# Kernel optimization log

Hardware: AMD Instinct MI355X
Metric: run time of the kernel (lower is better)

The kernel has to match this reference:

```python
import jax, jax.numpy as jnp
import numpy as np

IN, H, OUT = 128, 256, 128


def setup_inputs() -> dict:
    key = jax.random.key(0)
    ks = jax.random.split(key, 12)
    B, T = 32, 128
    s_in = 1.0 / np.sqrt(IN)
    s_h = 1.0 / np.sqrt(H)
    return {
        "x": jax.random.normal(ks[0], (B, T, IN), dtype=jnp.float32),
        "timespans": jax.random.uniform(ks[1], (B, T), dtype=jnp.float32),
        "tau_sys": jax.random.uniform(ks[2], (H,), dtype=jnp.float32) * 10.0 + 1.0,
        "sigma": jnp.ones((H,), dtype=jnp.float32) * 0.5,
        "W_A": jax.random.normal(ks[3], (H, H), dtype=jnp.float32) * s_h,
        "W_B": jax.random.normal(ks[4], (H, IN), dtype=jnp.float32) * s_in,
        "b_B": jax.random.normal(ks[5], (H,), dtype=jnp.float32) * s_in,
        "W_C": jax.random.normal(ks[6], (OUT, H), dtype=jnp.float32) * s_h,
        "b_C": jax.random.normal(ks[7], (OUT,), dtype=jnp.float32) * s_h,
        "W_ih": jax.random.normal(ks[8], (4 * H, IN), dtype=jnp.float32) * s_h,
        "W_hh": jax.random.normal(ks[9], (4 * H, H), dtype=jnp.float32) * s_h,
        "b_ih": jax.random.normal(ks[10], (4 * H,), dtype=jnp.float32) * s_h,
        "b_hh": jax.random.normal(ks[11], (4 * H,), dtype=jnp.float32) * s_h,
    }


def _lstm(x, W_ih, W_hh, b_ih, b_hh):
    # x: [B,T,IN] -> backbone_out: [B,T,H]; torch gate order i,f,g,o
    B = x.shape[0]
    xg = jnp.einsum("bti,gi->btg", x, W_ih) + b_ih  # precompute input contribution

    def step(carry, xg_t):
        h, c = carry
        gates = xg_t + h @ W_hh.T + b_hh
        i, f, g, o = jnp.split(gates, 4, axis=-1)
        c = jax.nn.sigmoid(f) * c + jax.nn.sigmoid(i) * jnp.tanh(g)
        h = jax.nn.sigmoid(o) * jnp.tanh(c)
        return (h, c), h

    h0 = jnp.zeros((B, H), dtype=x.dtype)
    c0 = jnp.zeros((B, H), dtype=x.dtype)
    _, hs = jax.lax.scan(step, (h0, c0), jnp.swapaxes(xg, 0, 1))
    return jnp.swapaxes(hs, 0, 1)  # [B,T,H]


def reference(x, timespans, tau_sys, sigma, W_A, W_B, b_B, W_C, b_C,
              W_ih, W_hh, b_ih, b_hh):
    B, T, _ = x.shape
    backbone_out = _lstm(x, W_ih, W_hh, b_ih, b_hh)  # [B,T,H]

    A_eff = W_A / tau_sys[None, :]        # [H,H] (divide columns, as in torch)
    I = jnp.eye(H, dtype=x.dtype)
    Bx = jnp.einsum("bti,hi->bth", x, W_B) + b_B  # precompute B(x_t) for all t

    def step(h, inp):
        x_t_Bx, bb_t, ts_t = inp  # [B,H], [B,H], [B]
        f_h = jnp.tanh(h / sigma)
        At = A_eff[None, :, :] * ts_t[:, None, None]            # [B,H,H]
        exp_At = I + At + 0.5 * jnp.einsum("bij,bjk->bik", At, At)
        h_new = jnp.einsum("bij,bj->bi", exp_At, h)
        drive = x_t_Bx + f_h @ W_A.T
        h_new = h_new + ts_t[:, None] * drive / tau_sys[None, :]
        h_new = h_new + bb_t
        y = h_new @ W_C.T + b_C
        return h_new, y

    h0 = jnp.zeros((B, H), dtype=x.dtype)
    xs = (jnp.swapaxes(Bx, 0, 1), jnp.swapaxes(backbone_out, 0, 1),
          jnp.swapaxes(timespans, 0, 1))
    _, ys = jax.lax.scan(step, h0, xs)
    return jnp.swapaxes(ys, 0, 1)  # [B,T,OUT]
```

## Files before the change

kernel.cpp:

```cpp
#include <hip/hip_runtime.h>
#include <math.h>

#define T_ 128

#define OFF_M2      0
#define OFF_WCOMBT  65536
#define OFF_BIAS    229376
#define OFF_WCT     230656
#define OFF_XG2     263424
#define OFF_BX2     4457728
#define OFF_HSEQ    5506304
#define OFF_HCSEQ   6554880

#define SENTB 0xFFFFFFFFu

typedef float f4 __attribute__((ext_vector_type(4)));

__device__ __forceinline__ float sigm_f(float x) { return 1.0f / (1.0f + __expf(-x)); }
__device__ __forceinline__ float tanh_f(float x) { return 1.0f - 2.0f / (__expf(2.0f * x) + 1.0f); }

__device__ __forceinline__ unsigned long long aload_u64(const unsigned long long* p) {
  return __hip_atomic_load(p, __ATOMIC_RELAXED, __HIP_MEMORY_SCOPE_AGENT);
}
__device__ __forceinline__ void astore_f(float* p, float v) {
  __hip_atomic_store(p, v, __ATOMIC_RELAXED, __HIP_MEMORY_SCOPE_AGENT);
}
__device__ __forceinline__ bool bad_u64(unsigned long long v) {
  return (unsigned)v == SENTB || (unsigned)(v >> 32) == SENTB;
}

__global__ __launch_bounds__(256) void prep_kernel(
    const float* __restrict__ W_ih, const float* __restrict__ W_B,
    const float* __restrict__ b_ih, const float* __restrict__ b_hh,
    const float* __restrict__ b_B,  const float* __restrict__ W_C,
    const float* __restrict__ W_A,  const float* __restrict__ tau,
    float* __restrict__ ws) {
  __shared__ float adrow[256];
  const int blk = blockIdx.x, tid = threadIdx.x;
  if (blk < 640) {
    const int idx = blk * 256 + tid;
    const int k = idx / 1280, c = idx - k * 1280;
    ws[OFF_WCOMBT + idx] = (c < 1024) ? W_ih[c * 128 + k] : W_B[(c - 1024) * 128 + k];
  } else if (blk == 640) {
#pragma unroll
    for (int i = 0; i < 5; ++i) {
      const int id = i * 256 + tid;
      ws[OFF_BIAS + id] = (id < 1024) ? (b_ih[id] + b_hh[id]) : b_B[id - 1024];
    }
  } else if (blk < 769) {
    const int idx = (blk - 641) * 256 + tid;
    const int k = idx >> 7, o = idx & 127;
    ws[OFF_WCT + idx] = W_C[o * 256 + k];
  } else if (blk < 1025) {
    const int i = blk - 769, k = tid;
    const float itk = 1.0f / tau[k];
    adrow[k] = W_A[i * 256 + k] * itk;
    __syncthreads();
    float s = 0.f;
#pragma unroll 8
    for (int m = 0; m < 256; ++m)
      s = fmaf(adrow[m], W_A[m * 256 + k], s);
    ws[OFF_M2 + i * 256 + k] = s * itk;
  } else {
    uint4* dst = (uint4*)(ws + OFF_HSEQ);
    const uint4 sv = make_uint4(SENTB, SENTB, SENTB, SENTB);
    const int tg = (blk - 1025) * 256 + tid;
#pragma unroll
    for (int i = 0; i < 16; ++i) dst[tg + i * 32768] = sv;
  }
}

__global__ __launch_bounds__(256) void xgt_kernel(
    const float* __restrict__ x, const float* __restrict__ WT,
    const float* __restrict__ bias, float* __restrict__ xg2,
    float* __restrict__ bx2) {
  __shared__ float xs[8 * 128];
  const int tid = threadIdx.x;
  const int rt = blockIdx.x, ct = blockIdx.y;
  ((float4*)xs)[tid] = ((const float4*)(x + rt * 1024))[tid];
  __syncthreads();
  const int r = tid >> 5, cg = tid & 31;
  const int c0 = ct * 256 + cg * 8;
  const float4* b4 = (const float4*)(bias + c0);
  float4 bA = b4[0], bB = b4[1];
  float a[8] = {bA.x, bA.y, bA.z, bA.w, bB.x, bB.y, bB.z, bB.w};
  const float4* xr4 = (const float4*)(xs + r * 128);
#pragma unroll 4
  for (int k4 = 0; k4 < 32; ++k4) {
    float4 xv = xr4[k4];
#define STEPB(kk, comp)                                                      \
    {                                                                        \
      const float4* w = (const float4*)(WT + (k4 * 4 + kk) * 1280 + c0);     \
      float4 wA = w[0], wB = w[1];                                           \
      a[0] = fmaf(wA.x, comp, a[0]); a[1] = fmaf(wA.y, comp, a[1]);          \
      a[2] = fmaf(wA.z, comp, a[2]); a[3] = fmaf(wA.w, comp, a[3]);          \
      a[4] = fmaf(wB.x, comp, a[4]); a[5] = fmaf(wB.y, comp, a[5]);          \
      a[6] = fmaf(wB.z, comp, a[6]); a[7] = fmaf(wB.w, comp, a[7]);          \
    }
    STEPB(0, xv.x) STEPB(1, xv.y) STEPB(2, xv.z) STEPB(3, xv.w)
#undef STEPB
  }
  const int row = rt * 8 + r;
  const int b = row >> 7, t = row & 127;
  if (ct < 4) {
    float* dst = xg2 + (size_t)(t * 32 + b) * 1024 + ct * 256 + cg * 8;
#pragma unroll
    for (int i = 0; i < 8; ++i) dst[i] = a[i];
  } else {
    float* dst = bx2 + (size_t)(t * 32 + b) * 256 + cg * 8;
#pragma unroll
    for (int i = 0; i < 8; ++i) dst[i] = a[i];
  }
}

__device__ __forceinline__ float wc_elem(
    const float* __restrict__ W_A, const float* __restrict__ M2,
    const float* __restrict__ tau, int ci, float it_i, int kp) {
  if (kp < 256)      return W_A[ci * 256 + kp] / tau[kp];
  else if (kp < 512) return W_A[ci * 256 + (kp - 256)] * it_i;
  else               return 0.5f * M2[ci * 256 + (kp - 512)];
}

__global__ __launch_bounds__(256, 4) void recur_bp_kernel(
    const float* __restrict__ ts_all, const float* __restrict__ tau,
    const float* __restrict__ sigma, const float* __restrict__ W_hh,
    const float* __restrict__ W_A, const float* __restrict__ M2,
    const float* __restrict__ xg2, const float* __restrict__ bx2,
    float* __restrict__ hseq, float* __restrict__ hcseq) {
  const int tid = threadIdx.x;
  const int lane = tid & 63, w = tid >> 6;
  const unsigned long long* hsq  = (const unsigned long long*)hseq;
  const unsigned long long* hcsq = (const unsigned long long*)hcseq;

  __shared__ float h_s[2][256];
  __shared__ float q_s[2][768];

  if (blockIdx.x < 512) {
    const int b = blockIdx.x >> 4, cb16 = blockIdx.x & 15;
    const int kq = lane & 3;
    const int gt = (lane >> 2) & 3;
    const int dim = cb16 * 16 + 4 * w + (lane >> 4);
    const int grow = gt * 256 + dim;
    const f4* wsrc = (const f4*)(W_hh + grow * 256);
    f4 wq0  = wsrc[0 * 4 + kq],  wq1  = wsrc[1 * 4 + kq];
    f4 wq2  = wsrc[2 * 4 + kq],  wq3  = wsrc[3 * 4 + kq];
    f4 wq4  = wsrc[4 * 4 + kq],  wq5  = wsrc[5 * 4 + kq];
    f4 wq6  = wsrc[6 * 4 + kq],  wq7  = wsrc[7 * 4 + kq];
    f4 wq8  = wsrc[8 * 4 + kq],  wq9  = wsrc[9 * 4 + kq];
    f4 wq10 = wsrc[10 * 4 + kq], wq11 = wsrc[11 * 4 + kq];
    f4 wq12 = wsrc[12 * 4 + kq], wq13 = wsrc[13 * 4 + kq];
    f4 wq14 = wsrc[14 * 4 + kq], wq15 = wsrc[15 * 4 + kq];
    asm volatile("" : "+v"(wq0), "+v"(wq1), "+v"(wq2), "+v"(wq3),
                      "+v"(wq4), "+v"(wq5), "+v"(wq6), "+v"(wq7),
                      "+v"(wq8), "+v"(wq9), "+v"(wq10), "+v"(wq11),
                      "+v"(wq12), "+v"(wq13), "+v"(wq14), "+v"(wq15));
    float c_reg = 0.f;
    const int dcol = dim;

    for (int t = 0; t < T_; ++t) {
      const int buf = t & 1;
      float xgi = 0.f, xgf = 0.f, xgg = 0.f, xgo = 0.f;
      if ((lane & 15) == 0) {
        const float* xp = xg2 + (size_t)(t * 32 + b) * 1024 + dcol;
        xgi = xp[0]; xgf = xp[256]; xgg = xp[512]; xgo = xp[768];
      }
      if (t == 0) {
        if (tid < 128) ((float2*)h_s[0])[tid] = make_float2(0.f, 0.f);
      } else if (tid < 128) {
        const unsigned long long* pp = hsq + (size_t)((t - 1) * 32 + b) * 128 + tid;
        unsigned long long v = aload_u64(pp);
        int spins = 0;
        while (bad_u64(v)) {
          if (++spins > 16) __builtin_amdgcn_s_sleep(1);
          v = aload_u64(pp);
        }
        union { unsigned long long u; float2 f; } H; H.u = v;
        ((float2*)h_s[buf])[tid] = H.f;
      }
      __syncthreads();

      const f4* h4 = (const f4*)h_s[buf];
      float s = 0.f;
#define LSTEP(i4, W)                                                         \
      {                                                                      \
        const f4 hv = h4[i4 * 4 + kq];                                       \
        s = fmaf(W.x, hv.x, s); s = fmaf(W.y, hv.y, s);                      \
        s = fmaf(W.z, hv.z, s); s = fmaf(W.w, hv.w, s);                      \
      }
      LSTEP(0, wq0)   LSTEP(1, wq1)   LSTEP(2, wq2)   LSTEP(3, wq3)
      LSTEP(4, wq4)   LSTEP(5, wq5)   LSTEP(6, wq6)   LSTEP(7, wq7)
      LSTEP(8, wq8)   LSTEP(9, wq9)   LSTEP(10, wq10) LSTEP(11, wq11)
      LSTEP(12, wq12) LSTEP(13, wq13) LSTEP(14, wq14) LSTEP(15, wq15)
#undef LSTEP
      s += __shfl_xor(s, 1); s += __shfl_xor(s, 2);
      const int base = lane & 48;
      const float gi = __shfl(s, base);
      const float gf = __shfl(s, base + 4);
      const float gg = __shfl(s, base + 8);
      const float go = __shfl(s, base + 12);
      if ((lane & 15) == 0) {
        const float i_ = sigm_f(gi + xgi);
        const float f_ = sigm_f(gf + xgf);
        const float g_ = tanh_f(gg + xgg);
        const float o_ = sigm_f(go + xgo);
        c_reg = fmaf(f_, c_reg, i_ * g_);
        const float ht = o_ * tanh_f(c_reg);
        astore_f(hseq + (size_t)(t * 32 + b) * 256 + dcol, ht);
      }
      (void)gt;
    }
  } else {
    const int bix = blockIdx.x - 512;
    const int b = bix >> 4, cb16 = bix & 15;
    const int r_in = lane >> 4, kq16 = lane & 15;
    const int ci = cb16 * 16 + 4 * w + r_in;
    const float it_i = 1.0f / tau[ci];
#define WCLOAD(i4)                                                           \
    (f4){wc_elem(W_A, M2, tau, ci, it_i, (i4 * 16 + kq16) * 4 + 0),          \
         wc_elem(W_A, M2, tau, ci, it_i, (i4 * 16 + kq16) * 4 + 1),          \
         wc_elem(W_A, M2, tau, ci, it_i, (i4 * 16 + kq16) * 4 + 2),          \
         wc_elem(W_A, M2, tau, ci, it_i, (i4 * 16 + kq16) * 4 + 3)}
    f4 wc0  = WCLOAD(0),  wc1  = WCLOAD(1),  wc2  = WCLOAD(2);
    f4 wc3  = WCLOAD(3),  wc4  = WCLOAD(4),  wc5  = WCLOAD(5);
    f4 wc6  = WCLOAD(6),  wc7  = WCLOAD(7),  wc8  = WCLOAD(8);
    f4 wc9  = WCLOAD(9),  wc10 = WCLOAD(10), wc11 = WCLOAD(11);
#undef WCLOAD
    asm volatile("" : "+v"(wc0), "+v"(wc1), "+v"(wc2), "+v"(wc3),
                      "+v"(wc4), "+v"(wc5), "+v"(wc6), "+v"(wc7),
                      "+v"(wc8), "+v"(wc9), "+v"(wc10), "+v"(wc11));
    float2 isg2 = make_float2(0.f, 0.f);
    if (tid < 128) isg2 = make_float2(1.0f / sigma[2 * tid], 1.0f / sigma[2 * tid + 1]);
    const bool fin = (kq16 == 0);

    for (int t = 0; t < T_; ++t) {
      const int buf = t & 1;
      const float ts = ts_all[b * T_ + t];
      float bx_v = 0.f;
      if (fin) bx_v = bx2[(size_t)(t * 32 + b) * 256 + ci];

      if (t == 0) {
        if (tid < 128) {
          const float2 z = make_float2(0.f, 0.f);
          ((float2*)h_s[0])[tid] = z;
          float2* qrow = (float2*)q_s[0];
          qrow[tid] = z; qrow[128 + tid] = z; qrow[256 + tid] = z;
        }
      } else if (tid < 128) {
        const size_t base = (size_t)((t - 1) * 32 + b) * 128 + tid;
        const unsigned long long* pc = hcsq + base;
        const unsigned long long* ph = hsq + base;
        unsigned long long vc = aload_u64(pc);
        unsigned long long vh = aload_u64(ph);
        int spins = 0;
        while (bad_u64(vc) || bad_u64(vh)) {
          if (++spins > 16) __builtin_amdgcn_s_sleep(1);
          vc = aload_u64(pc);
          vh = aload_u64(ph);
        }
        union { unsigned long long u; float2 f; } C, H;
        C.u = vc; H.u = vh;
        const float2 hcv = make_float2(C.f.x + H.f.x, C.f.y + H.f.y);
        ((float2*)h_s[buf])[tid] = hcv;
        float2* qrow = (float2*)q_s[buf];
        qrow[tid]       = make_float2(ts * hcv.x, ts * hcv.y);
        qrow[128 + tid] = make_float2(ts * tanh_f(hcv.x * isg2.x),
                                      ts * tanh_f(hcv.y * isg2.y));
        qrow[256 + tid] = make_float2(ts * (ts * hcv.x), ts * (ts * hcv.y));
      }
      __syncthreads();

      const f4* q4 = (const f4*)q_s[buf];
      float s = 0.f;
#define CSTEP(i4, W)                                                         \
      {                                                                      \
        const f4 qv = q4[i4 * 16 + kq16];                                    \
        s = fmaf(W.x, qv.x, s); s = fmaf(W.y, qv.y, s);                      \
        s = fmaf(W.z, qv.z, s); s = fmaf(W.w, qv.w, s);                      \
      }
      CSTEP(0, wc0)  CSTEP(1, wc1)  CSTEP(2, wc2)  CSTEP(3, wc3)
      CSTEP(4, wc4)  CSTEP(5, wc5)  CSTEP(6, wc6)  CSTEP(7, wc7)
      CSTEP(8, wc8)  CSTEP(9, wc9)  CSTEP(10, wc10) CSTEP(11, wc11)
#undef CSTEP
      s += __shfl_xor(s, 1); s += __shfl_xor(s, 2);
      s += __shfl_xor(s, 4); s += __shfl_xor(s, 8);
      if (fin) {
        const float hc_own = h_s[buf][ci];
        const float hn_p = hc_own + s + ts * bx_v * it_i;
        astore_f(hcseq + (size_t)(t * 32 + b) * 256 + ci, hn_p);
      }
      (void)r_in;
    }
  }
}

__global__ __launch_bounds__(256) void out_kernel(
    const float* __restrict__ hc, const float* __restrict__ ht,
    const float* __restrict__ WCT, const float* __restrict__ bC,
    float* __restrict__ y) {
  __shared__ float hs[16 * 256];
  const int tid = threadIdx.x;
#pragma unroll
  for (int v = 0; v < 4; ++v) {
    const int flat = v * 256 + tid;
    const int r = flat >> 6, f4i = flat & 63;
    const int row = blockIdx.x * 16 + r;
    const int b = row >> 7, t = row & 127;
    const float4 a = ((const float4*)(hc + (size_t)(t * 32 + b) * 256))[f4i];
    const float4 h = ((const float4*)(ht + (size_t)(t * 32 + b) * 256))[f4i];
    ((float4*)hs)[flat] = make_float4(a.x + h.x, a.y + h.y, a.z + h.z, a.w + h.w);
  }
  __syncthreads();
  const int r = tid >> 4, cgg = tid & 15;
  const int c0 = cgg * 8;
  const float4* b4 = (const float4*)(bC + c0);
  float4 bA = b4[0], bB = b4[1];
  float a0 = bA.x, a1 = bA.y, a2 = bA.z, a3 = bA.w;
  float a4 = bB.x, a5 = bB.y, a6 = bB.z, a7 = bB.w;
  const float4* hr4 = (const float4*)(hs + r * 256);
#pragma unroll 4
  for (int k4 = 0; k4 < 64; ++k4) {
    float4 hv = hr4[k4];
#define STEPD(kk, comp)                                                     \
    {                                                                       \
      const float4* w = (const float4*)(WCT + (k4 * 4 + kk) * 128 + c0);    \
      float4 wA = w[0], wB = w[1];                                          \
      a0 = fmaf(wA.x, comp, a0); a1 = fmaf(wA.y, comp, a1);                 \
      a2 = fmaf(wA.z, comp, a2); a3 = fmaf(wA.w, comp, a3);                 \
      a4 = fmaf(wB.x, comp, a4); a5 = fmaf(wB.y, comp, a5);                 \
      a6 = fmaf(wB.z, comp, a6); a7 = fmaf(wB.w, comp, a7);                 \
    }
    STEPD(0, hv.x) STEPD(1, hv.y) STEPD(2, hv.z) STEPD(3, hv.w)
#undef STEPD
  }
  const int row = blockIdx.x * 16 + r;
  float4* dst = (float4*)(y + (size_t)row * 128 + c0);
  dst[0] = make_float4(a0, a1, a2, a3);
  dst[1] = make_float4(a4, a5, a6, a7);
}

extern "C" void kernel_launch(void* const* d_in, const int* in_sizes, int n_in,
                              void* d_out, int out_size, void* d_ws, size_t ws_size,
                              hipStream_t stream) {
  const float* x     = (const float*)d_in[0];
  const float* tspan = (const float*)d_in[1];
  const float* tau   = (const float*)d_in[2];
  const float* sigma = (const float*)d_in[3];
  const float* W_A   = (const float*)d_in[4];
  const float* W_B   = (const float*)d_in[5];
  const float* b_B   = (const float*)d_in[6];
  const float* W_C   = (const float*)d_in[7];
  const float* b_C   = (const float*)d_in[8];
  const float* W_ih  = (const float*)d_in[9];
  const float* W_hh  = (const float*)d_in[10];
  const float* b_ih  = (const float*)d_in[11];
  const float* b_hh  = (const float*)d_in[12];
  float* ws = (float*)d_ws;
  float* y = (float*)d_out;

  prep_kernel<<<1153, 256, 0, stream>>>(W_ih, W_B, b_ih, b_hh, b_B, W_C,
                                        W_A, tau, ws);
  xgt_kernel<<<dim3(512, 5), 256, 0, stream>>>(x, ws + OFF_WCOMBT, ws + OFF_BIAS,
                                               ws + OFF_XG2, ws + OFF_BX2);
  recur_bp_kernel<<<1024, 256, 0, stream>>>(
      tspan, tau, sigma, W_hh, W_A, ws + OFF_M2, ws + OFF_XG2, ws + OFF_BX2,
      ws + OFF_HSEQ, ws + OFF_HCSEQ);
  out_kernel<<<256, 256, 0, stream>>>(ws + OFF_HCSEQ, ws + OFF_HSEQ,
                                      ws + OFF_WCT, b_C, y);
}
```

Before: 409.6 us.

## Fuse output projection into recurrent kernel and register-tile input GEMM

The separate output-projection kernel is removed. Each of the 1024 recurrent blocks now spins on sentinel-tagged hseq/hcseq entries for four rows once its recurrent work finishes, sums them, and computes y for those rows in place, hiding the tail kernel launch and overlapping the projection with the ongoing recurrence. The input-projection kernel is also changed to compute four rows per thread with vectorized stores, cutting grid size and weight reloads. The fused tail adds spin-waiting inside blocks that may still be needed for the recurrence, which risks contention or delay.

```diff
diff --git a/kernel.cpp b/kernel.cpp
--- a/kernel.cpp
+++ b/kernel.cpp
@@ -74,42 +74,58 @@
     const float* __restrict__ x, const float* __restrict__ WT,
     const float* __restrict__ bias, float* __restrict__ xg2,
     float* __restrict__ bx2) {
-  __shared__ float xs[8 * 128];
+  __shared__ float xs[32 * 128];
   const int tid = threadIdx.x;
   const int rt = blockIdx.x, ct = blockIdx.y;
-  ((float4*)xs)[tid] = ((const float4*)(x + rt * 1024))[tid];
+  {
+    const float4* src4 = (const float4*)(x + (size_t)rt * 4096);
+    float4* d4 = (float4*)xs;
+#pragma unroll
+    for (int v = 0; v < 4; ++v) d4[v * 256 + tid] = src4[v * 256 + tid];
+  }
   __syncthreads();
-  const int r = tid >> 5, cg = tid & 31;
+  const int rg = tid >> 5, cg = tid & 31;
   const int c0 = ct * 256 + cg * 8;
   const float4* b4 = (const float4*)(bias + c0);
-  float4 bA = b4[0], bB = b4[1];
-  float a[8] = {bA.x, bA.y, bA.z, bA.w, bB.x, bB.y, bB.z, bB.w};
-  const float4* xr4 = (const float4*)(xs + r * 128);
-#pragma unroll 4
+  const float4 bA = b4[0], bB = b4[1];
+  float a[4][8];
+#pragma unroll
+  for (int i = 0; i < 4; ++i) {
+    a[i][0] = bA.x; a[i][1] = bA.y; a[i][2] = bA.z; a[i][3] = bA.w;
+    a[i][4] = bB.x; a[i][5] = bB.y; a[i][6] = bB.z; a[i][7] = bB.w;
+  }
+  const float4* xr0 = (const float4*)(xs + (rg * 4 + 0) * 128);
+  const float4* xr1 = (const float4*)(xs + (rg * 4 + 1) * 128);
+  const float4* xr2 = (const float4*)(xs + (rg * 4 + 2) * 128);
+  const float4* xr3 = (const float4*)(xs + (rg * 4 + 3) * 128);
+#pragma unroll 2
   for (int k4 = 0; k4 < 32; ++k4) {
-    float4 xv = xr4[k4];
-#define STEPB(kk, comp)                                                      \
-    {                                                                        \
-      const float4* w = (const float4*)(WT + (k4 * 4 + kk) * 1280 + c0);     \
-      float4 wA = w[0], wB = w[1];                                           \
-      a[0] = fmaf(wA.x, comp, a[0]); a[1] = fmaf(wA.y, comp, a[1]);          \
-      a[2] = fmaf(wA.z, comp, a[2]); a[3] = fmaf(wA.w, comp, a[3]);          \
-      a[4] = fmaf(wB.x, comp, a[4]); a[5] = fmaf(wB.y, comp, a[5]);          \
-      a[6] = fmaf(wB.z, comp, a[6]); a[7] = fmaf(wB.w, comp, a[7]);          \
-    }
-    STEPB(0, xv.x) STEPB(1, xv.y) STEPB(2, xv.z) STEPB(3, xv.w)
-#undef STEPB
-  }
-  const int row = rt * 8 + r;
-  const int b = row >> 7, t = row & 127;
-  if (ct < 4) {
-    float* dst = xg2 + (size_t)(t * 32 + b) * 1024 + ct * 256 + cg * 8;
-#pragma unroll
-    for (int i = 0; i < 8; ++i) dst[i] = a[i];
-  } else {
-    float* dst = bx2 + (size_t)(t * 32 + b) * 256 + cg * 8;
-#pragma unroll
-    for (int i = 0; i < 8; ++i) dst[i] = a[i];
+    const float4 xv0 = xr0[k4], xv1 = xr1[k4], xv2 = xr2[k4], xv3 = xr3[k4];
+    const float xk[4][4] = {
+        {xv0.x, xv0.y, xv0.z, xv0.w}, {xv1.x, xv1.y, xv1.z, xv1.w},
+        {xv2.x, xv2.y, xv2.z, xv2.w}, {xv3.x, xv3.y, xv3.z, xv3.w}};
+#pragma unroll
+    for (int kk = 0; kk < 4; ++kk) {
+      const float4* wp = (const float4*)(WT + (k4 * 4 + kk) * 1280 + c0);
+      const float4 wA = wp[0], wB = wp[1];
+      const float wv[8] = {wA.x, wA.y, wA.z, wA.w, wB.x, wB.y, wB.z, wB.w};
+#pragma unroll
+      for (int i = 0; i < 4; ++i)
+#pragma unroll
+        for (int j = 0; j < 8; ++j)
+          a[i][j] = fmaf(wv[j], xk[i][kk], a[i][j]);
+    }
+  }
+#pragma unroll
+  for (int i = 0; i < 4; ++i) {
+    const int row = rt * 32 + rg * 4 + i;
+    const int b = row >> 7, t = row & 127;
+    float* dst = (ct < 4)
+        ? xg2 + (size_t)(t * 32 + b) * 1024 + ct * 256 + cg * 8
+        : bx2 + (size_t)(t * 32 + b) * 256 + cg * 8;
+    float4* d4 = (float4*)dst;
+    d4[0] = make_float4(a[i][0], a[i][1], a[i][2], a[i][3]);
+    d4[1] = make_float4(a[i][4], a[i][5], a[i][6], a[i][7]);
   }
 }
 
@@ -126,7 +142,9 @@
     const float* __restrict__ sigma, const float* __restrict__ W_hh,
     const float* __restrict__ W_A, const float* __restrict__ M2,
     const float* __restrict__ xg2, const float* __restrict__ bx2,
-    float* __restrict__ hseq, float* __restrict__ hcseq) {
+    float* __restrict__ hseq, float* __restrict__ hcseq,
+    const float* __restrict__ WCT, const float* __restrict__ bC,
+    float* __restrict__ y) {
   const int tid = threadIdx.x;
   const int lane = tid & 63, w = tid >> 6;
   const unsigned long long* hsq  = (const unsigned long long*)hseq;
@@ -291,51 +309,54 @@
       (void)r_in;
     }
   }
-}
-
-__global__ __launch_bounds__(256) void out_kernel(
-    const float* __restrict__ hc, const float* __restrict__ ht,
-    const float* __restrict__ WCT, const float* __restrict__ bC,
-    float* __restrict__ y) {
-  __shared__ float hs[16 * 256];
-  const int tid = threadIdx.x;
-#pragma unroll
-  for (int v = 0; v < 4; ++v) {
-    const int flat = v * 256 + tid;
-    const int r = flat >> 6, f4i = flat & 63;
-    const int row = blockIdx.x * 16 + r;
-    const int b = row >> 7, t = row & 127;
-    const float4 a = ((const float4*)(hc + (size_t)(t * 32 + b) * 256))[f4i];
-    const float4 h = ((const float4*)(ht + (size_t)(t * 32 + b) * 256))[f4i];
-    ((float4*)hs)[flat] = make_float4(a.x + h.x, a.y + h.y, a.z + h.z, a.w + h.w);
-  }
+
   __syncthreads();
-  const int r = tid >> 4, cgg = tid & 15;
-  const int c0 = cgg * 8;
-  const float4* b4 = (const float4*)(bC + c0);
-  float4 bA = b4[0], bB = b4[1];
-  float a0 = bA.x, a1 = bA.y, a2 = bA.z, a3 = bA.w;
-  float a4 = bB.x, a5 = bB.y, a6 = bB.z, a7 = bB.w;
-  const float4* hr4 = (const float4*)(hs + r * 256);
+  {
+    float* ys = &q_s[0][0];
+    if (tid < 128) {
+      size_t bases[4];
+#pragma unroll
+      for (int i = 0; i < 4; ++i) {
+        const int row = 4 * (int)blockIdx.x + i;
+        const int bb = row >> 7, tt = row & 127;
+        bases[i] = (size_t)(tt * 32 + bb) * 128 + tid;
+      }
+      unsigned long long vc[4], vh[4];
+      bool again; int spins = 0;
+      do {
+        again = false;
+#pragma unroll
+        for (int i = 0; i < 4; ++i) {
+          vc[i] = aload_u64(hcsq + bases[i]);
+          vh[i] = aload_u64(hsq + bases[i]);
+        }
+#pragma unroll
+        for (int i = 0; i < 4; ++i)
+          if (bad_u64(vc[i]) || bad_u64(vh[i])) again = true;
+        if (again && ++spins > 16) __builtin_amdgcn_s_sleep(1);
+      } while (again);
+#pragma unroll
+      for (int i = 0; i < 4; ++i) {
+        union { unsigned long long u; float2 f; } C, H;
+        C.u = vc[i]; H.u = vh[i];
+        ((float2*)(ys + i * 256))[tid] =
+            make_float2(C.f.x + H.f.x, C.f.y + H.f.y);
+      }
+    }
+    __syncthreads();
+    const int row = 4 * (int)blockIdx.x + w;
+    const float2* bc2 = (const float2*)bC;
+    float2 acc = bc2[lane];
+    const float* yrow = ys + w * 256;
 #pragma unroll 4
-  for (int k4 = 0; k4 < 64; ++k4) {
-    float4 hv = hr4[k4];
-#define STEPD(kk, comp)                                                     \
-    {                                                                       \
-      const float4* w = (const float4*)(WCT + (k4 * 4 + kk) * 128 + c0);    \
-      float4 wA = w[0], wB = w[1];                                          \
-      a0 = fmaf(wA.x, comp, a0); a1 = fmaf(wA.y, comp, a1);                 \
-      a2 = fmaf(wA.z, comp, a2); a3 = fmaf(wA.w, comp, a3);                 \
-      a4 = fmaf(wB.x, comp, a4); a5 = fmaf(wB.y, comp, a5);                 \
-      a6 = fmaf(wB.z, comp, a6); a7 = fmaf(wB.w, comp, a7);                 \
-    }
-    STEPD(0, hv.x) STEPD(1, hv.y) STEPD(2, hv.z) STEPD(3, hv.w)
-#undef STEPD
-  }
-  const int row = blockIdx.x * 16 + r;
-  float4* dst = (float4*)(y + (size_t)row * 128 + c0);
-  dst[0] = make_float4(a0, a1, a2, a3);
-  dst[1] = make_float4(a4, a5, a6, a7);
+    for (int k = 0; k < 256; ++k) {
+      const float hv = yrow[k];
+      const float2 wv = ((const float2*)(WCT + k * 128))[lane];
+      acc.x = fmaf(wv.x, hv, acc.x);
+      acc.y = fmaf(wv.y, hv, acc.y);
+    }
+    ((float2*)(y + (size_t)row * 128))[lane] = acc;
+  }
 }
 
 extern "C" void kernel_launch(void* const* d_in, const int* in_sizes, int n_in,
@@ -359,11 +380,9 @@
 
   prep_kernel<<<1153, 256, 0, stream>>>(W_ih, W_B, b_ih, b_hh, b_B, W_C,
                                         W_A, tau, ws);
-  xgt_kernel<<<dim3(512, 5), 256, 0, stream>>>(x, ws + OFF_WCOMBT, ws + OFF_BIAS,
+  xgt_kernel<<<dim3(128, 5), 256, 0, stream>>>(x, ws + OFF_WCOMBT, ws + OFF_BIAS,
                                                ws + OFF_XG2, ws + OFF_BX2);
   recur_bp_kernel<<<1024, 256, 0, stream>>>(
       tspan, tau, sigma, W_hh, W_A, ws + OFF_M2, ws + OFF_XG2, ws + OFF_BX2,
-      ws + OFF_HSEQ, ws + OFF_HCSEQ);
-  out_kernel<<<256, 256, 0, stream>>>(ws + OFF_HCSEQ, ws + OFF_HSEQ,
-                                      ws + OFF_WCT, b_C, y);
-}
+      ws + OFF_HSEQ, ws + OFF_HCSEQ, ws + OFF_WCT, b_C, y);
+}
```

New measurement: 368.9 us. 1.11x faster.
